# Kernel optimization log

Measured on AMD Instinct MI355X. Metric: run time of the kernel, lower is better.

## Reference

```python
import jax, jax.numpy as jnp
import numpy as np

B, T, E, H = 64, 512, 512, 512


def setup_inputs() -> dict:
    key = jax.random.key(0)
    ks = jax.random.split(key, 10)
    s = 1.0 / np.sqrt(H)  # torch GRU init: U(-1/sqrt(H), 1/sqrt(H))
    u = lambda k, shape: jax.random.uniform(k, shape, jnp.float32, -s, s)
    return {
        "xs": jax.random.normal(ks[0], (B, T, E), jnp.float32),
        "w_ih0": u(ks[1], (2, 3 * H, E)),
        "w_hh0": u(ks[2], (2, 3 * H, H)),
        "b_ih0": u(ks[3], (2, 3 * H)),
        "b_hh0": u(ks[4], (2, 3 * H)),
        "w_ih1": u(ks[5], (2, 3 * H, 2 * H)),
        "w_hh1": u(ks[6], (2, 3 * H, H)),
        "b_ih1": u(ks[7], (2, 3 * H)),
        "b_hh1": u(ks[8], (2, 3 * H)),
    }


def _gru_dir(x, w_ih, w_hh, b_ih, b_hh):
    # x: [B, T, D]; returns hs [B, T, H], h_T [B, H]
    h_dim = w_hh.shape[1]
    gx = jnp.einsum("btd,gd->btg", x, w_ih) + b_ih  # [B, T, 3H], all input GEMMs batched

    def step(h, gx_t):
        gh = h @ w_hh.T + b_hh
        r = jax.nn.sigmoid(gx_t[:, :h_dim] + gh[:, :h_dim])
        z = jax.nn.sigmoid(gx_t[:, h_dim:2 * h_dim] + gh[:, h_dim:2 * h_dim])
        n = jnp.tanh(gx_t[:, 2 * h_dim:] + r * gh[:, 2 * h_dim:])
        h = (1.0 - z) * n + z * h
        return h, h

    h0 = jnp.zeros((x.shape[0], h_dim), x.dtype)
    hT, hs = jax.lax.scan(step, h0, jnp.swapaxes(gx, 0, 1))
    return jnp.swapaxes(hs, 0, 1), hT


def _bidir_layer(x, w_ih, w_hh, b_ih, b_hh):
    hs_f, h_f = _gru_dir(x, w_ih[0], w_hh[0], b_ih[0], b_hh[0])
    hs_b, h_b = _gru_dir(x[:, ::-1], w_ih[1], w_hh[1], b_ih[1], b_hh[1])
    hs_b = hs_b[:, ::-1]
    return jnp.concatenate([hs_f, hs_b], axis=-1), jnp.stack([h_f, h_b])


def reference(xs, w_ih0, w_hh0, b_ih0, b_hh0, w_ih1, w_hh1, b_ih1, b_hh1):
    h0_out, hy0 = _bidir_layer(xs, w_ih0, w_hh0, b_ih0, b_hh0)
    h1_out, hy1 = _bidir_layer(h0_out, w_ih1, w_hh1, b_ih1, b_hh1)
    hy = jnp.concatenate([hy0, hy1], axis=0)  # [n_layers*2, B, H]
    # dropout p=0.0 -> identity
    return (h1_out, hy)
```

## Files before the change

### kernel.cpp

```cpp
#include <hip/hip_runtime.h>
#include <stdint.h>

#define Bq 64
#define Tq 512
#define Hq 512
#define G3 1536

typedef unsigned short u16;
typedef uint32_t u32;
typedef unsigned long long u64;
typedef __attribute__((ext_vector_type(8))) short bf16x8;
typedef __attribute__((ext_vector_type(4))) float f32x4;

__device__ __forceinline__ float bf2f(u16 v){ unsigned u = ((unsigned)v)<<16; float f; __builtin_memcpy(&f,&u,4); return f; }
__device__ __forceinline__ u16 f2bf(float f){ unsigned u; __builtin_memcpy(&u,&f,4); u += 0x7fffu + ((u>>16)&1u); return (u16)(u>>16); }

__global__ void detect_k(const u16* __restrict__ xs, int* __restrict__ flag){
  __shared__ int cnt;
  if (threadIdx.x==0) cnt = 0;
  __syncthreads();
  int good = 0;
  for (int i = threadIdx.x; i < 4096; i += 256) {
    u16 v = xs[2*i];
    int e = (v>>7)&0xFF;
    if (e==0 || (e>=100 && e<=140)) good++;
  }
  atomicAdd(&cnt, good);
  __syncthreads();
  if (threadIdx.x==0) flag[0] = (cnt > 3600) ? 1 : 0;
}

template<int K, int AMODE, int OUTF32>
__global__ __launch_bounds__(256,1) void gemm_gx(const void* __restrict__ Araw,
        const void* __restrict__ Wraw, const void* __restrict__ braw,
        void* __restrict__ outraw, const int* __restrict__ dflag)
{
  __shared__ __align__(16) u16 Ah[64*72];
  __shared__ __align__(16) u16 Al[64*72];
  __shared__ __align__(16) u16 Wh[64*72];
  __shared__ __align__(16) u16 Wl[64*72];
  const int bf16in = dflag[0];
  const bool useAlo = (AMODE==0) && !bf16in;
  const bool useWlo = !bf16in;
  const int dir = blockIdx.z;
  const int tid = threadIdx.x;
  const int m0 = blockIdx.x*64, n0 = blockIdx.y*64;
  const int wave = tid>>6, lane = tid&63;
  const int wm = (wave>>1)*32, wn = (wave&1)*32;
  f32x4 acc[2][2] = {};

  for (int kb=0; kb<K/64; kb++) {
    if (AMODE==0 && !bf16in) {
      const float* Af = (const float*)Araw;
      #pragma unroll
      for (int it=0; it<4; it++) {
        int c = it*256 + tid;
        int r = c>>4, cc = (c&15)*4;
        float4 v = *(const float4*)&Af[(size_t)(m0+r)*K + kb*64 + cc];
        u16 h0=f2bf(v.x), h1=f2bf(v.y), h2=f2bf(v.z), h3=f2bf(v.w);
        *(ushort4*)&Ah[r*72+cc] = make_ushort4(h0,h1,h2,h3);
        *(ushort4*)&Al[r*72+cc] = make_ushort4(
            f2bf(v.x-bf2f(h0)), f2bf(v.y-bf2f(h1)),
            f2bf(v.z-bf2f(h2)), f2bf(v.w-bf2f(h3)));
      }
    } else {
      const u16* Ab = (const u16*)Araw;
      #pragma unroll
      for (int it=0; it<2; it++) {
        int c = it*256 + tid;
        int r = c>>3, cc = (c&7)*8;
        *(bf16x8*)&Ah[r*72+cc] = *(const bf16x8*)&Ab[(size_t)(m0+r)*K + kb*64 + cc];
      }
    }
    if (!bf16in) {
      const float* Wf = (const float*)Wraw + (size_t)dir*G3*K;
      #pragma unroll
      for (int it=0; it<4; it++) {
        int c = it*256 + tid;
        int r = c>>4, cc = (c&15)*4;
        float4 v = *(const float4*)&Wf[(size_t)(n0+r)*K + kb*64 + cc];
        u16 h0=f2bf(v.x), h1=f2bf(v.y), h2=f2bf(v.z), h3=f2bf(v.w);
        *(ushort4*)&Wh[r*72+cc] = make_ushort4(h0,h1,h2,h3);
        *(ushort4*)&Wl[r*72+cc] = make_ushort4(
            f2bf(v.x-bf2f(h0)), f2bf(v.y-bf2f(h1)),
            f2bf(v.z-bf2f(h2)), f2bf(v.w-bf2f(h3)));
      }
    } else {
      const u16* Wb = (const u16*)Wraw + (size_t)dir*G3*K;
      #pragma unroll
      for (int it=0; it<2; it++) {
        int c = it*256 + tid;
        int r = c>>3, cc = (c&7)*8;
        *(bf16x8*)&Wh[r*72+cc] = *(const bf16x8*)&Wb[(size_t)(n0+r)*K + kb*64 + cc];
      }
    }
    __syncthreads();
    #pragma unroll
    for (int ks=0; ks<2; ks++) {
      int ko = ks*32 + (lane>>4)*8;
      bf16x8 a0 = *(const bf16x8*)&Ah[(wm    + (lane&15))*72 + ko];
      bf16x8 a1 = *(const bf16x8*)&Ah[(wm+16 + (lane&15))*72 + ko];
      bf16x8 b0 = *(const bf16x8*)&Wh[(wn    + (lane&15))*72 + ko];
      bf16x8 b1 = *(const bf16x8*)&Wh[(wn+16 + (lane&15))*72 + ko];
      acc[0][0] = __builtin_amdgcn_mfma_f32_16x16x32_bf16(a0,b0,acc[0][0],0,0,0);
      acc[0][1] = __builtin_amdgcn_mfma_f32_16x16x32_bf16(a0,b1,acc[0][1],0,0,0);
      acc[1][0] = __builtin_amdgcn_mfma_f32_16x16x32_bf16(a1,b0,acc[1][0],0,0,0);
      acc[1][1] = __builtin_amdgcn_mfma_f32_16x16x32_bf16(a1,b1,acc[1][1],0,0,0);
      if (useAlo) {
        bf16x8 c0 = *(const bf16x8*)&Al[(wm    + (lane&15))*72 + ko];
        bf16x8 c1 = *(const bf16x8*)&Al[(wm+16 + (lane&15))*72 + ko];
        acc[0][0] = __builtin_amdgcn_mfma_f32_16x16x32_bf16(c0,b0,acc[0][0],0,0,0);
        acc[0][1] = __builtin_amdgcn_mfma_f32_16x16x32_bf16(c0,b1,acc[0][1],0,0,0);
        acc[1][0] = __builtin_amdgcn_mfma_f32_16x16x32_bf16(c1,b0,acc[1][0],0,0,0);
        acc[1][1] = __builtin_amdgcn_mfma_f32_16x16x32_bf16(c1,b1,acc[1][1],0,0,0);
      }
      if (useWlo) {
        bf16x8 d0 = *(const bf16x8*)&Wl[(wn    + (lane&15))*72 + ko];
        bf16x8 d1 = *(const bf16x8*)&Wl[(wn+16 + (lane&15))*72 + ko];
        acc[0][0] = __builtin_amdgcn_mfma_f32_16x16x32_bf16(a0,d0,acc[0][0],0,0,0);
        acc[0][1] = __builtin_amdgcn_mfma_f32_16x16x32_bf16(a0,d1,acc[0][1],0,0,0);
        acc[1][0] = __builtin_amdgcn_mfma_f32_16x16x32_bf16(a1,d0,acc[1][0],0,0,0);
        acc[1][1] = __builtin_amdgcn_mfma_f32_16x16x32_bf16(a1,d1,acc[1][1],0,0,0);
      }
    }
    __syncthreads();
  }
  #pragma unroll
  for (int i=0;i<2;i++) {
    #pragma unroll
    for (int j=0;j<2;j++) {
      int nn = n0 + wn + j*16 + (lane&15);
      float bv = bf16in ? bf2f(((const u16*)braw)[dir*G3 + nn])
                        : ((const float*)braw)[dir*G3 + nn];
      #pragma unroll
      for (int r=0;r<4;r++) {
        int mm = m0 + wm + i*16 + (lane>>4)*4 + r;
        int b = mm >> 9, t = mm & 511;
        size_t oi = ((size_t)(dir*Tq + t)*Bq + b)*G3 + nn;
        float v = acc[i][j][r] + bv;
        if (OUTF32) ((float*)outraw)[oi] = v;
        else        ((u16*)outraw)[oi]   = f2bf(v);
      }
    }
  }
}

template<int LAYER, int GXF32>
__global__ __launch_bounds__(384,1) void gru_scan(const void* __restrict__ whh,
        const void* __restrict__ bhh, const void* __restrict__ gx,
        u16* __restrict__ hs0, void* __restrict__ dout,
        u32* __restrict__ hexw, int* __restrict__ flags,
        const int* __restrict__ dflag)
{
  extern __shared__ char smem[];
  u16*   wlds = (u16*)smem;
  u16*   ht   = (u16*)(smem + 99840);
  u32*   htw  = (u32*)ht;

  const int bf16in = dflag[0];
  const int tid = threadIdx.x;
  const int bx  = blockIdx.x;
  const int dir = bx>>6, group=(bx>>4)&3, slice=bx&15;
  const int jbase = slice*32, bg0 = group*16;
  int* fl = flags + (dir*4+group)*16;

  if (!bf16in) {
    const float* wf = (const float*)whh + (size_t)dir*G3*Hq;
    for (int c = tid; c < 96*128; c += 384) {
      int r = c>>7, q = (c&127)*4;
      int gate = r>>5, jj = r&31;
      float4 v = *(const float4*)&wf[(size_t)(gate*512 + jbase + jj)*Hq + q];
      *(ushort4*)&wlds[r*520 + q] = make_ushort4(f2bf(v.x),f2bf(v.y),f2bf(v.z),f2bf(v.w));
    }
  } else {
    const u16* wb = (const u16*)whh + (size_t)dir*G3*Hq;
    for (int c = tid; c < 96*64; c += 384) {
      int r = c>>6, cc = (c&63)*8;
      int gate = r>>5, jj = r&31;
      *(bf16x8*)&wlds[r*520 + cc] = *(const bf16x8*)&wb[(size_t)(gate*512 + jbase + jj)*Hq + cc];
    }
  }
  __syncthreads();

  const int wave = tid>>6, lane = tid&63;
  const bool cw = (wave < 2);
  const int j0 = wave*16 + (lane&15);
  const int bq = (lane>>4)*4;

  float bR=0.f, bZ=0.f, bN=0.f;
  if (cw) {
    int off = dir*G3 + jbase + j0;
    if (bf16in) { const u16* bb=(const u16*)bhh;
      bR=bf2f(bb[off]); bZ=bf2f(bb[off+512]); bN=bf2f(bb[off+1024]); }
    else { const float* bb=(const float*)bhh;
      bR=bb[off]; bZ=bb[off+512]; bN=bb[off+1024]; }
  }

  float h[4] = {0.f,0.f,0.f,0.f};
  float gxr[4], gxz[4], gxn[4];
  auto ldgx = [&](int t_in_){
    #pragma unroll
    for (int i=0;i<4;i++){
      size_t gb = ((size_t)(dir*Tq + t_in_)*Bq + (bg0 + bq + i))*G3 + jbase + j0;
      if (GXF32) { const float* gp=(const float*)gx + gb;
        gxr[i]=gp[0]; gxz[i]=gp[512]; gxn[i]=gp[1024]; }
      else { const u16* gp=(const u16*)gx + gb;
        gxr[i]=bf2f(gp[0]); gxz[i]=bf2f(gp[512]); gxn[i]=bf2f(gp[1024]); }
    }
  };
  if (cw) ldgx(dir ? (Tq-1) : 0);

  for (int s=0; s<Tq; s++) {
    const int t_in = dir ? (Tq-1-s) : s;
    if (tid < 16) {
      while (__hip_atomic_fetch_add(&fl[tid], 0, __ATOMIC_RELAXED, __HIP_MEMORY_SCOPE_AGENT) < 2*s) {
        __builtin_amdgcn_s_sleep(1);
      }
    }
    __syncthreads();
    {
      const u32 rb = (u32)(((s&1)*2 + dir)*Bq + bg0)*256u;
      for (int c = tid; c < 16*128; c += 384) {
        int r = c>>7, w2 = c&127;
        u64 v = __hip_atomic_fetch_add((u64*)&hexw[rb + (u32)r*256u + (u32)(2*w2)],
                                  (u64)0, __ATOMIC_RELAXED, __HIP_MEMORY_SCOPE_AGENT);
        *(u64*)&htw[r*260 + 2*w2] = v;
      }
    }
    __syncthreads();

    if (cw) {
      f32x4 aR = {0.f,0.f,0.f,0.f}, aZ = {0.f,0.f,0.f,0.f}, aN = {0.f,0.f,0.f,0.f};
      const int wl = wave*16 + (lane&15);
      #pragma unroll
      for (int kk=0; kk<16; kk++) {
        int ko = kk*32 + (lane>>4)*8;
        bf16x8 a  = *(const bf16x8*)&ht[(lane&15)*520 + ko];
        bf16x8 b0 = *(const bf16x8*)&wlds[(     wl)*520 + ko];
        bf16x8 b1 = *(const bf16x8*)&wlds[(32 + wl)*520 + ko];
        bf16x8 b2 = *(const bf16x8*)&wlds[(64 + wl)*520 + ko];
        aR = __builtin_amdgcn_mfma_f32_16x16x32_bf16(a,b0,aR,0,0,0);
        aZ = __builtin_amdgcn_mfma_f32_16x16x32_bf16(a,b1,aZ,0,0,0);
        aN = __builtin_amdgcn_mfma_f32_16x16x32_bf16(a,b2,aN,0,0,0);
      }
      const u32 rb2 = (u32)((((s+1)&1)*2 + dir)*Bq + bg0)*256u;
      u16 hb[4]; float hn[4];
      #pragma unroll
      for (int i=0;i<4;i++) {
        float rr = gxr[i] + aR[i] + bR;
        float zz = gxz[i] + aZ[i] + bZ;
        float gh =          aN[i] + bN;
        float r = 1.f/(1.f + __expf(-rr));
        float z = 1.f/(1.f + __expf(-zz));
        float x = gxn[i] + r*gh;
        x = fminf(fmaxf(x, -15.f), 15.f);
        float e2 = __expf(2.f*x);
        float n = (e2 - 1.f)/(e2 + 1.f);
        hn[i] = (1.f - z)*n + z*h[i];
        h[i] = hn[i]; hb[i] = f2bf(hn[i]);
      }
      #pragma unroll
      for (int i=0;i<4;i++) {
        u32 p1 = (u32)__shfl_down((int)hb[i], 1);
        u32 p2 = (u32)__shfl_down((int)hb[i], 2);
        u32 p3 = (u32)__shfl_down((int)hb[i], 3);
        if ((lane & 3) == 0) {
          u64 pk = (u64)hb[i] | ((u64)(p1 & 0xffffu) << 16)
                 | ((u64)(p2 & 0xffffu) << 32) | ((u64)(p3 & 0xffffu) << 48);
          (void)__hip_atomic_exchange((u64*)&hexw[rb2 + (u32)(bq+i)*256u + (u32)(slice*16 + (j0>>1))],
                                      pk, __ATOMIC_RELAXED, __HIP_MEMORY_SCOPE_AGENT);
        }
      }
      asm volatile("s_waitcnt vmcnt(0)" ::: "memory");
      if (lane == 0) {
        (void)__hip_atomic_fetch_add(&fl[slice], 1, __ATOMIC_RELAXED, __HIP_MEMORY_SCOPE_AGENT);
      }
      if (s+1 < Tq) ldgx(dir ? (Tq-2-s) : (s+1));
      #pragma unroll
      for (int i=0;i<4;i++) {
        int bg = bg0 + bq + i;
        size_t oi = ((size_t)bg*Tq + t_in)*1024 + dir*512 + jbase + j0;
        if (LAYER==0) {
          __builtin_nontemporal_store(hb[i], &hs0[oi]);
        } else {
          if (bf16in) __builtin_nontemporal_store(hb[i], &((u16*)dout)[oi]);
          else        __builtin_nontemporal_store(hn[i], &((float*)dout)[oi]);
        }
        if (s == Tq-1) {
          size_t hyi = (size_t)Bq*Tq*1024 + ((size_t)(LAYER*2 + dir)*Bq + bg)*512 + jbase + j0;
          if (bf16in) ((u16*)dout)[hyi] = hb[i];
          else        ((float*)dout)[hyi] = hn[i];
        }
      }
    }
  }
}

__global__ void init_k(u32* hexw, int* flags){
  int i = blockIdx.x*256 + threadIdx.x;
  if (i < 2*2*Bq*256) hexw[i] = 0;
  if (i < 128) flags[i] = 0;
}

extern "C" void kernel_launch(void* const* d_in, const int* in_sizes, int n_in,
                              void* d_out, int out_size, void* d_ws, size_t ws_size,
                              hipStream_t stream)
{
  const void* xs    = d_in[0];
  const void* w_ih0 = d_in[1];
  const void* w_hh0 = d_in[2];
  const void* b_ih0 = d_in[3];
  const void* b_hh0 = d_in[4];
  const void* w_ih1 = d_in[5];
  const void* w_hh1 = d_in[6];
  const void* b_ih1 = d_in[7];
  const void* b_hh1 = d_in[8];
  (void)in_sizes; (void)n_in; (void)out_size;

  char* ws   = (char*)d_ws;
  int* dflag = (int*)ws;
  int* flags = (int*)(ws + 256);
  u32* hexw  = (u32*)(ws + 1024);
  void* gx   = (void*)(ws + 263168ULL);
  const bool gxf32 = ws_size >= 263168ULL + 402653184ULL;
  u16* hs0   = (u16*)d_out;

  hipFuncSetAttribute((const void*)gru_scan<0,0>, hipFuncAttributeMaxDynamicSharedMemorySize, 116480);
  hipFuncSetAttribute((const void*)gru_scan<1,0>, hipFuncAttributeMaxDynamicSharedMemorySize, 116480);
  hipFuncSetAttribute((const void*)gru_scan<0,1>, hipFuncAttributeMaxDynamicSharedMemorySize, 116480);
  hipFuncSetAttribute((const void*)gru_scan<1,1>, hipFuncAttributeMaxDynamicSharedMemorySize, 116480);

  dim3 gg(Tq*Bq/64, G3/64, 2);

  detect_k<<<1, 256, 0, stream>>>((const u16*)xs, dflag);
  init_k<<<512, 256, 0, stream>>>(hexw, flags);
  if (gxf32) {
    gemm_gx<512,0,1><<<gg, 256, 0, stream>>>(xs, w_ih0, b_ih0, gx, dflag);
    gru_scan<0,1><<<128, 384, 116480, stream>>>(w_hh0, b_hh0, gx, hs0, d_out, hexw, flags, dflag);
    gemm_gx<1024,1,1><<<gg, 256, 0, stream>>>(hs0, w_ih1, b_ih1, gx, dflag);
    init_k<<<512, 256, 0, stream>>>(hexw, flags);
    gru_scan<1,1><<<128, 384, 116480, stream>>>(w_hh1, b_hh1, gx, hs0, d_out, hexw, flags, dflag);
  } else {
    gemm_gx<512,0,0><<<gg, 256, 0, stream>>>(xs, w_ih0, b_ih0, gx, dflag);
    gru_scan<0,0><<<128, 384, 116480, stream>>>(w_hh0, b_hh0, gx, hs0, d_out, hexw, flags, dflag);
    gemm_gx<1024,1,0><<<gg, 256, 0, stream>>>(hs0, w_ih1, b_ih1, gx, dflag);
    init_k<<<512, 256, 0, stream>>>(hexw, flags);
    gru_scan<1,0><<<128, 384, 116480, stream>>>(w_hh1, b_hh1, gx, hs0, d_out, hexw, flags, dflag);
  }
}
```

Baseline: 6.283 ms.

## Collapse GRU scan step to a single wave loading h directly into registers

The recurrent scan block shrinks from 384 threads (two compute waves plus helper waves) to one compute wave that covers both 16-column halves. Each step now reads the exchanged hidden state from global memory straight into MFMA operand registers, instead of staging it in LDS behind two block barriers. This removes the __syncthreads and the LDS round-trip from the serial critical path, and the flag target drops from 2*s to s because each block now publishes once per step. In exchange the wave does twice the MFMA and elementwise work per step and holds about 64 more registers for the loaded h.

Result: no change. 6.200 ms (-1.3%).

```diff
diff --git a/kernel.cpp b/kernel.cpp
--- a/kernel.cpp
+++ b/kernel.cpp
@@ -146,16 +146,14 @@
 }
 
 template<int LAYER, int GXF32>
-__global__ __launch_bounds__(384,1) void gru_scan(const void* __restrict__ whh,
+__global__ __launch_bounds__(128,1) void gru_scan(const void* __restrict__ whh,
         const void* __restrict__ bhh, const void* __restrict__ gx,
         u16* __restrict__ hs0, void* __restrict__ dout,
         u32* __restrict__ hexw, int* __restrict__ flags,
         const int* __restrict__ dflag)
 {
   extern __shared__ char smem[];
-  u16*   wlds = (u16*)smem;
-  u16*   ht   = (u16*)(smem + 99840);
-  u32*   htw  = (u32*)ht;
+  u16* wlds = (u16*)smem;
 
   const int bf16in = dflag[0];
   const int tid = threadIdx.x;
@@ -166,7 +164,7 @@
 
   if (!bf16in) {
     const float* wf = (const float*)whh + (size_t)dir*G3*Hq;
-    for (int c = tid; c < 96*128; c += 384) {
+    for (int c = tid; c < 96*128; c += 128) {
       int r = c>>7, q = (c&127)*4;
       int gate = r>>5, jj = r&31;
       float4 v = *(const float4*)&wf[(size_t)(gate*512 + jbase + jj)*Hq + q];
@@ -174,123 +172,133 @@
     }
   } else {
     const u16* wb = (const u16*)whh + (size_t)dir*G3*Hq;
-    for (int c = tid; c < 96*64; c += 384) {
+    for (int c = tid; c < 96*64; c += 128) {
       int r = c>>6, cc = (c&63)*8;
       int gate = r>>5, jj = r&31;
       *(bf16x8*)&wlds[r*520 + cc] = *(const bf16x8*)&wb[(size_t)(gate*512 + jbase + jj)*Hq + cc];
     }
   }
   __syncthreads();
-
-  const int wave = tid>>6, lane = tid&63;
-  const bool cw = (wave < 2);
-  const int j0 = wave*16 + (lane&15);
+  if (tid >= 64) return;
+
+  const int lane = tid;
+  const int j0 = lane&15;
   const int bq = (lane>>4)*4;
 
-  float bR=0.f, bZ=0.f, bN=0.f;
-  if (cw) {
-    int off = dir*G3 + jbase + j0;
+  float bR[2], bZ[2], bN[2];
+  #pragma unroll
+  for (int c=0;c<2;c++) {
+    int off = dir*G3 + jbase + c*16 + j0;
     if (bf16in) { const u16* bb=(const u16*)bhh;
-      bR=bf2f(bb[off]); bZ=bf2f(bb[off+512]); bN=bf2f(bb[off+1024]); }
+      bR[c]=bf2f(bb[off]); bZ[c]=bf2f(bb[off+512]); bN[c]=bf2f(bb[off+1024]); }
     else { const float* bb=(const float*)bhh;
-      bR=bb[off]; bZ=bb[off+512]; bN=bb[off+1024]; }
-  }
-
-  float h[4] = {0.f,0.f,0.f,0.f};
-  float gxr[4], gxz[4], gxn[4];
+      bR[c]=bb[off]; bZ[c]=bb[off+512]; bN[c]=bb[off+1024]; }
+  }
+
+  float h[2][4] = {};
+  float gxr[2][4], gxz[2][4], gxn[2][4];
   auto ldgx = [&](int t_in_){
     #pragma unroll
+    for (int c=0;c<2;c++)
+    #pragma unroll
     for (int i=0;i<4;i++){
-      size_t gb = ((size_t)(dir*Tq + t_in_)*Bq + (bg0 + bq + i))*G3 + jbase + j0;
+      size_t gb = ((size_t)(dir*Tq + t_in_)*Bq + (bg0 + bq + i))*G3 + jbase + c*16 + j0;
       if (GXF32) { const float* gp=(const float*)gx + gb;
-        gxr[i]=gp[0]; gxz[i]=gp[512]; gxn[i]=gp[1024]; }
+        gxr[c][i]=gp[0]; gxz[c][i]=gp[512]; gxn[c][i]=gp[1024]; }
       else { const u16* gp=(const u16*)gx + gb;
-        gxr[i]=bf2f(gp[0]); gxz[i]=bf2f(gp[512]); gxn[i]=bf2f(gp[1024]); }
+        gxr[c][i]=bf2f(gp[0]); gxz[c][i]=bf2f(gp[512]); gxn[c][i]=bf2f(gp[1024]); }
     }
   };
-  if (cw) ldgx(dir ? (Tq-1) : 0);
+  ldgx(dir ? (Tq-1) : 0);
 
   for (int s=0; s<Tq; s++) {
     const int t_in = dir ? (Tq-1-s) : s;
-    if (tid < 16) {
-      while (__hip_atomic_fetch_add(&fl[tid], 0, __ATOMIC_RELAXED, __HIP_MEMORY_SCOPE_AGENT) < 2*s) {
+    if (lane < 16) {
+      while (__hip_atomic_fetch_add(&fl[lane], 0, __ATOMIC_RELAXED, __HIP_MEMORY_SCOPE_AGENT) < s) {
         __builtin_amdgcn_s_sleep(1);
       }
     }
-    __syncthreads();
-    {
-      const u32 rb = (u32)(((s&1)*2 + dir)*Bq + bg0)*256u;
-      for (int c = tid; c < 16*128; c += 384) {
-        int r = c>>7, w2 = c&127;
-        u64 v = __hip_atomic_fetch_add((u64*)&hexw[rb + (u32)r*256u + (u32)(2*w2)],
-                                  (u64)0, __ATOMIC_RELAXED, __HIP_MEMORY_SCOPE_AGENT);
-        *(u64*)&htw[r*260 + 2*w2] = v;
-      }
-    }
-    __syncthreads();
-
-    if (cw) {
-      f32x4 aR = {0.f,0.f,0.f,0.f}, aZ = {0.f,0.f,0.f,0.f}, aN = {0.f,0.f,0.f,0.f};
-      const int wl = wave*16 + (lane&15);
-      #pragma unroll
-      for (int kk=0; kk<16; kk++) {
-        int ko = kk*32 + (lane>>4)*8;
-        bf16x8 a  = *(const bf16x8*)&ht[(lane&15)*520 + ko];
+    asm volatile("" ::: "memory");
+    const u32 rb = (u32)(((s&1)*2 + dir)*Bq + bg0)*256u;
+    u64 areg[32];
+    #pragma unroll
+    for (int kk=0; kk<16; kk++) {
+      u32 base = rb + (u32)(lane&15)*256u + (u32)(kk*16 + (lane>>4)*4);
+      areg[2*kk]   = __hip_atomic_fetch_add((u64*)&hexw[base],   (u64)0, __ATOMIC_RELAXED, __HIP_MEMORY_SCOPE_AGENT);
+      areg[2*kk+1] = __hip_atomic_fetch_add((u64*)&hexw[base+2], (u64)0, __ATOMIC_RELAXED, __HIP_MEMORY_SCOPE_AGENT);
+    }
+    f32x4 aR[2] = {{0.f,0.f,0.f,0.f},{0.f,0.f,0.f,0.f}};
+    f32x4 aZ[2] = {{0.f,0.f,0.f,0.f},{0.f,0.f,0.f,0.f}};
+    f32x4 aN[2] = {{0.f,0.f,0.f,0.f},{0.f,0.f,0.f,0.f}};
+    #pragma unroll
+    for (int kk=0; kk<16; kk++) {
+      union { u64 q[2]; bf16x8 v; } ab;
+      ab.q[0] = areg[2*kk]; ab.q[1] = areg[2*kk+1];
+      int ko = kk*32 + (lane>>4)*8;
+      #pragma unroll
+      for (int c=0;c<2;c++) {
+        int wl = c*16 + j0;
         bf16x8 b0 = *(const bf16x8*)&wlds[(     wl)*520 + ko];
         bf16x8 b1 = *(const bf16x8*)&wlds[(32 + wl)*520 + ko];
         bf16x8 b2 = *(const bf16x8*)&wlds[(64 + wl)*520 + ko];
-        aR = __builtin_amdgcn_mfma_f32_16x16x32_bf16(a,b0,aR,0,0,0);
-        aZ = __builtin_amdgcn_mfma_f32_16x16x32_bf16(a,b1,aZ,0,0,0);
-        aN = __builtin_amdgcn_mfma_f32_16x16x32_bf16(a,b2,aN,0,0,0);
-      }
-      const u32 rb2 = (u32)((((s+1)&1)*2 + dir)*Bq + bg0)*256u;
-      u16 hb[4]; float hn[4];
-      #pragma unroll
-      for (int i=0;i<4;i++) {
-        float rr = gxr[i] + aR[i] + bR;
-        float zz = gxz[i] + aZ[i] + bZ;
-        float gh =          aN[i] + bN;
-        float r = 1.f/(1.f + __expf(-rr));
-        float z = 1.f/(1.f + __expf(-zz));
-        float x = gxn[i] + r*gh;
-        x = fminf(fmaxf(x, -15.f), 15.f);
-        float e2 = __expf(2.f*x);
-        float n = (e2 - 1.f)/(e2 + 1.f);
-        hn[i] = (1.f - z)*n + z*h[i];
-        h[i] = hn[i]; hb[i] = f2bf(hn[i]);
-      }
-      #pragma unroll
-      for (int i=0;i<4;i++) {
-        u32 p1 = (u32)__shfl_down((int)hb[i], 1);
-        u32 p2 = (u32)__shfl_down((int)hb[i], 2);
-        u32 p3 = (u32)__shfl_down((int)hb[i], 3);
-        if ((lane & 3) == 0) {
-          u64 pk = (u64)hb[i] | ((u64)(p1 & 0xffffu) << 16)
-                 | ((u64)(p2 & 0xffffu) << 32) | ((u64)(p3 & 0xffffu) << 48);
-          (void)__hip_atomic_exchange((u64*)&hexw[rb2 + (u32)(bq+i)*256u + (u32)(slice*16 + (j0>>1))],
-                                      pk, __ATOMIC_RELAXED, __HIP_MEMORY_SCOPE_AGENT);
-        }
-      }
-      asm volatile("s_waitcnt vmcnt(0)" ::: "memory");
-      if (lane == 0) {
-        (void)__hip_atomic_fetch_add(&fl[slice], 1, __ATOMIC_RELAXED, __HIP_MEMORY_SCOPE_AGENT);
-      }
-      if (s+1 < Tq) ldgx(dir ? (Tq-2-s) : (s+1));
-      #pragma unroll
-      for (int i=0;i<4;i++) {
-        int bg = bg0 + bq + i;
-        size_t oi = ((size_t)bg*Tq + t_in)*1024 + dir*512 + jbase + j0;
-        if (LAYER==0) {
-          __builtin_nontemporal_store(hb[i], &hs0[oi]);
-        } else {
-          if (bf16in) __builtin_nontemporal_store(hb[i], &((u16*)dout)[oi]);
-          else        __builtin_nontemporal_store(hn[i], &((float*)dout)[oi]);
-        }
-        if (s == Tq-1) {
-          size_t hyi = (size_t)Bq*Tq*1024 + ((size_t)(LAYER*2 + dir)*Bq + bg)*512 + jbase + j0;
-          if (bf16in) ((u16*)dout)[hyi] = hb[i];
-          else        ((float*)dout)[hyi] = hn[i];
-        }
+        aR[c] = __builtin_amdgcn_mfma_f32_16x16x32_bf16(ab.v,b0,aR[c],0,0,0);
+        aZ[c] = __builtin_amdgcn_mfma_f32_16x16x32_bf16(ab.v,b1,aZ[c],0,0,0);
+        aN[c] = __builtin_amdgcn_mfma_f32_16x16x32_bf16(ab.v,b2,aN[c],0,0,0);
+      }
+    }
+    const u32 rb2 = (u32)((((s+1)&1)*2 + dir)*Bq + bg0)*256u;
+    u16 hb[2][4]; float hn[2][4];
+    #pragma unroll
+    for (int c=0;c<2;c++)
+    #pragma unroll
+    for (int i=0;i<4;i++) {
+      float rr = gxr[c][i] + aR[c][i] + bR[c];
+      float zz = gxz[c][i] + aZ[c][i] + bZ[c];
+      float gh =             aN[c][i] + bN[c];
+      float r = 1.f/(1.f + __expf(-rr));
+      float z = 1.f/(1.f + __expf(-zz));
+      float x = gxn[c][i] + r*gh;
+      x = fminf(fmaxf(x, -15.f), 15.f);
+      float e2 = __expf(2.f*x);
+      float n = (e2 - 1.f)/(e2 + 1.f);
+      hn[c][i] = (1.f - z)*n + z*h[c][i];
+      h[c][i] = hn[c][i]; hb[c][i] = f2bf(hn[c][i]);
+    }
+    #pragma unroll
+    for (int c=0;c<2;c++)
+    #pragma unroll
+    for (int i=0;i<4;i++) {
+      u32 p1 = (u32)__shfl_down((int)hb[c][i], 1);
+      u32 p2 = (u32)__shfl_down((int)hb[c][i], 2);
+      u32 p3 = (u32)__shfl_down((int)hb[c][i], 3);
+      if ((lane & 3) == 0) {
+        u64 pk = (u64)hb[c][i] | ((u64)(p1 & 0xffffu) << 16)
+               | ((u64)(p2 & 0xffffu) << 32) | ((u64)(p3 & 0xffffu) << 48);
+        (void)__hip_atomic_exchange((u64*)&hexw[rb2 + (u32)(bq+i)*256u + (u32)(slice*16 + c*8 + (j0>>1))],
+                                    pk, __ATOMIC_RELAXED, __HIP_MEMORY_SCOPE_AGENT);
+      }
+    }
+    asm volatile("s_waitcnt vmcnt(0)" ::: "memory");
+    if (lane == 0) {
+      (void)__hip_atomic_fetch_add(&fl[slice], 1, __ATOMIC_RELAXED, __HIP_MEMORY_SCOPE_AGENT);
+    }
+    if (s+1 < Tq) ldgx(dir ? (Tq-2-s) : (s+1));
+    #pragma unroll
+    for (int c=0;c<2;c++)
+    #pragma unroll
+    for (int i=0;i<4;i++) {
+      int bg = bg0 + bq + i;
+      size_t oi = ((size_t)bg*Tq + t_in)*1024 + dir*512 + jbase + c*16 + j0;
+      if (LAYER==0) {
+        __builtin_nontemporal_store(hb[c][i], &hs0[oi]);
+      } else {
+        if (bf16in) __builtin_nontemporal_store(hb[c][i], &((u16*)dout)[oi]);
+        else        __builtin_nontemporal_store(hn[c][i], &((float*)dout)[oi]);
+      }
+      if (s == Tq-1) {
+        size_t hyi = (size_t)Bq*Tq*1024 + ((size_t)(LAYER*2 + dir)*Bq + bg)*512 + jbase + c*16 + j0;
+        if (bf16in) ((u16*)dout)[hyi] = hb[c][i];
+        else        ((float*)dout)[hyi] = hn[c][i];
       }
     }
   }
@@ -325,10 +333,10 @@
   const bool gxf32 = ws_size >= 263168ULL + 402653184ULL;
   u16* hs0   = (u16*)d_out;
 
-  hipFuncSetAttribute((const void*)gru_scan<0,0>, hipFuncAttributeMaxDynamicSharedMemorySize, 116480);
-  hipFuncSetAttribute((const void*)gru_scan<1,0>, hipFuncAttributeMaxDynamicSharedMemorySize, 116480);
-  hipFuncSetAttribute((const void*)gru_scan<0,1>, hipFuncAttributeMaxDynamicSharedMemorySize, 116480);
-  hipFuncSetAttribute((const void*)gru_scan<1,1>, hipFuncAttributeMaxDynamicSharedMemorySize, 116480);
+  hipFuncSetAttribute((const void*)gru_scan<0,0>, hipFuncAttributeMaxDynamicSharedMemorySize, 99840);
+  hipFuncSetAttribute((const void*)gru_scan<1,0>, hipFuncAttributeMaxDynamicSharedMemorySize, 99840);
+  hipFuncSetAttribute((const void*)gru_scan<0,1>, hipFuncAttributeMaxDynamicSharedMemorySize, 99840);
+  hipFuncSetAttribute((const void*)gru_scan<1,1>, hipFuncAttributeMaxDynamicSharedMemorySize, 99840);
 
   dim3 gg(Tq*Bq/64, G3/64, 2);
 
@@ -336,15 +344,15 @@
   init_k<<<512, 256, 0, stream>>>(hexw, flags);
   if (gxf32) {
     gemm_gx<512,0,1><<<gg, 256, 0, stream>>>(xs, w_ih0, b_ih0, gx, dflag);
-    gru_scan<0,1><<<128, 384, 116480, stream>>>(w_hh0, b_hh0, gx, hs0, d_out, hexw, flags, dflag);
+    gru_scan<0,1><<<128, 128, 99840, stream>>>(w_hh0, b_hh0, gx, hs0, d_out, hexw, flags, dflag);
     gemm_gx<1024,1,1><<<gg, 256, 0, stream>>>(hs0, w_ih1, b_ih1, gx, dflag);
     init_k<<<512, 256, 0, stream>>>(hexw, flags);
-    gru_scan<1,1><<<128, 384, 116480, stream>>>(w_hh1, b_hh1, gx, hs0, d_out, hexw, flags, dflag);
+    gru_scan<1,1><<<128, 128, 99840, stream>>>(w_hh1, b_hh1, gx, hs0, d_out, hexw, flags, dflag);
   } else {
     gemm_gx<512,0,0><<<gg, 256, 0, stream>>>(xs, w_ih0, b_ih0, gx, dflag);
-    gru_scan<0,0><<<128, 384, 116480, stream>>>(w_hh0, b_hh0, gx, hs0, d_out, hexw, flags, dflag);
+    gru_scan<0,0><<<128, 128, 99840, stream>>>(w_hh0, b_hh0, gx, hs0, d_out, hexw, flags, dflag);
     gemm_gx<1024,1,0><<<gg, 256, 0, stream>>>(hs0, w_ih1, b_ih1, gx, dflag);
     init_k<<<512, 256, 0, stream>>>(hexw, flags);
-    gru_scan<1,0><<<128, 384, 116480, stream>>>(w_hh1, b_hh1, gx, hs0, d_out, hexw, flags, dflag);
-  }
-}
+    gru_scan<1,0><<<128, 128, 99840, stream>>>(w_hh1, b_hh1, gx, hs0, d_out, hexw, flags, dflag);
+  }
+}
```
